# Performance work log

Measured on AMD Instinct MI355X. Metric: run time of the kernel, lower is better.

Reference implementation:

```python
import jax, jax.numpy as jnp
import numpy as np

B, S, D = 2, 2048, 1024
HEADS, HEAD_DIM = 16, 64

def setup_inputs() -> dict:
    key = jax.random.key(0)
    ks = jax.random.split(key, 5)
    sc = 0.02
    return {
        "hidden_states": jax.random.normal(ks[0], (B, S, D), jnp.float32),
        "Wq": jax.random.normal(ks[1], (D, HEADS * HEAD_DIM), jnp.float32) * sc,
        "Wk": jax.random.normal(ks[2], (D, HEADS * HEAD_DIM), jnp.float32) * sc,
        "Wv": jax.random.normal(ks[3], (D, HEADS * HEAD_DIM), jnp.float32) * sc,
        "Wo": jax.random.normal(ks[4], (HEADS * HEAD_DIM, D), jnp.float32) * sc,
        "bo": jnp.zeros((D,), jnp.float32),
    }

def reference(hidden_states, Wq, Wk, Wv, Wo, bo):
    b, s, _ = hidden_states.shape
    # QKV projections (no bias, as in diffusers Attention defaults)
    q = (hidden_states @ Wq).reshape(b, s, HEADS, HEAD_DIM).transpose(0, 2, 1, 3)
    k = (hidden_states @ Wk).reshape(b, s, HEADS, HEAD_DIM).transpose(0, 2, 1, 3)
    v = (hidden_states @ Wv).reshape(b, s, HEADS, HEAD_DIM).transpose(0, 2, 1, 3)
    scale = 1.0 / jnp.sqrt(jnp.asarray(HEAD_DIM, hidden_states.dtype))
    scores = jnp.einsum('bhqd,bhkd->bhqk', q, k) * scale  # full NxN scores
    attn = jax.nn.softmax(scores, axis=-1)
    out = jnp.einsum('bhqk,bhkd->bhqd', attn, v)
    out = out.transpose(0, 2, 1, 3).reshape(b, s, HEADS * HEAD_DIM)
    return out @ Wo + bo
```

## Files before the change

### kernel.cpp

```cpp
#include <hip/hip_runtime.h>

#define B_ 2
#define S_ 2048
#define D_ 1024
#define H_ 16
#define HD_ 64
#define M_ (B_ * S_)

typedef __attribute__((ext_vector_type(4))) float f32x4;
typedef __attribute__((ext_vector_type(16))) float f32x16;
typedef __attribute__((ext_vector_type(8))) short s16x8;
typedef unsigned short u16;
typedef unsigned int u32;

#define QSCALE 0.1803368801111204f

__device__ __forceinline__ u16 f2bf(float f) {
  unsigned u = __float_as_uint(f);
  u += 0x7fffu + ((u >> 16) & 1u);
  return (u16)(u >> 16);
}

__device__ __forceinline__ u32 cvtpk_bf16(float lo, float hi) {
  u32 r;
  asm("v_cvt_pk_bf16_f32 %0, %1, %2" : "=v"(r) : "v"(lo), "v"(hi));
  return r;
}

__device__ __forceinline__ void g2lds16(const u16* g, u16* l) {
  __builtin_amdgcn_global_load_lds((const __attribute__((address_space(1))) u32*)(g),
                                   (__attribute__((address_space(3))) u32*)(l), 16, 0, 0);
}

__global__ __launch_bounds__(256) void prep_kernel(
    const float* __restrict__ X, const float* __restrict__ Wq,
    const float* __restrict__ Wk, const float* __restrict__ Wv,
    const float* __restrict__ Wo, u16* __restrict__ Xb, u16* __restrict__ Wt0) {
  __shared__ float tile[32][33];
  const int id = blockIdx.x;
  if (id < 4096) {
    int i = (id * 256 + threadIdx.x) * 4;
    const float4 v = *(const float4*)(X + i);
    ushort4 o;
    o.x = f2bf(v.x); o.y = f2bf(v.y); o.z = f2bf(v.z); o.w = f2bf(v.w);
    *(ushort4*)(Xb + i) = o;
    return;
  }
  const int id2 = id - 4096;
  const int z = id2 >> 10;
  const float* W = (z == 0) ? Wq : (z == 1) ? Wk : (z == 2) ? Wv : Wo;
  u16* Wt = Wt0 + (size_t)z * (D_ * D_);
  const float sc = (z == 0) ? QSCALE : 1.0f;
  const int tx = threadIdx.x & 31, ty = threadIdx.x >> 5;
  const int c0 = (id2 & 31) * 32, r0 = ((id2 >> 5) & 31) * 32;
#pragma unroll
  for (int j = 0; j < 32; j += 8)
    tile[ty + j][tx] = W[(size_t)(r0 + ty + j) * D_ + c0 + tx];
  __syncthreads();
#pragma unroll
  for (int j = 0; j < 32; j += 8)
    Wt[(size_t)(c0 + ty + j) * D_ + r0 + tx] = f2bf(tile[tx][ty + j] * sc);
}

__global__ __launch_bounds__(256) void gemm_qkv_kernel(
    const u16* __restrict__ Xb, const u16* __restrict__ WqT,
    const u16* __restrict__ WkT, const u16* __restrict__ WvT,
    u16* __restrict__ Qb, u16* __restrict__ Kb, u16* __restrict__ Vt) {
  __shared__ u16 As[2][128 * 32];
  __shared__ u16 Bs[2][128 * 32];
  const int tid = threadIdx.x;
  const int lane = tid & 63, wid = tid >> 6;
  const int wr = wid >> 1, wc = wid & 1;
  const int l15 = lane & 15, l4 = lane >> 4;
  const int bm = blockIdx.x * 128;
  const int bn128 = blockIdx.y;
  const int sel = bn128 >> 3;
  const u16* Wt = (sel == 0) ? WqT : (sel == 1) ? WkT : WvT;
  const int bn = (bn128 & 7) * 128;
  const int r0 = lane >> 2;
  const int c0 = lane & 3;

#define GSTAGE(buf, kt)                                                          \
  do {                                                                           \
    _Pragma("unroll") for (int j = 0; j < 2; ++j) {                              \
      const int row = (wid * 2 + j) * 16 + r0;                                   \
      g2lds16(Xb + (size_t)(bm + row) * D_ + (kt) + c0 * 8,                      \
              &As[buf][(wid * 2 + j) * 512]);                                    \
      g2lds16(Wt + (size_t)(bn + row) * D_ + (kt) + c0 * 8,                      \
              &Bs[buf][(wid * 2 + j) * 512]);                                    \
    }                                                                            \
  } while (0)

  f32x4 acc[4][4] = {};
  GSTAGE(0, 0);
  __syncthreads();
  int cur = 0;
  for (int kt = 0; kt < D_; kt += 32) {
    GSTAGE(cur ^ 1, (kt + 32) & (D_ - 1));
    s16x8 af[4], bfr[4];
#pragma unroll
    for (int i = 0; i < 4; ++i) af[i] = *(const s16x8*)&As[cur][(wr * 64 + i * 16 + l15) * 32 + l4 * 8];
#pragma unroll
    for (int j = 0; j < 4; ++j) bfr[j] = *(const s16x8*)&Bs[cur][(wc * 64 + j * 16 + l15) * 32 + l4 * 8];
#pragma unroll
    for (int i = 0; i < 4; ++i)
#pragma unroll
      for (int j = 0; j < 4; ++j)
        acc[i][j] = __builtin_amdgcn_mfma_f32_16x16x32_bf16(af[i], bfr[j], acc[i][j], 0, 0, 0);
    __syncthreads();
    cur ^= 1;
  }
#undef GSTAGE
#pragma unroll
  for (int i = 0; i < 4; ++i)
#pragma unroll
    for (int j = 0; j < 4; ++j)
#pragma unroll
      for (int r = 0; r < 4; ++r) {
        int m = bm + wr * 64 + i * 16 + l4 * 4 + r;
        int n = bn + wc * 64 + j * 16 + l15;
        int bb = m >> 11, s = m & (S_ - 1);
        int h = n >> 6, d = n & 63;
        u16 v = f2bf(acc[i][j][r]);
        size_t bhsel = (size_t)bb * H_ + h;
        if (sel == 0)      Qb[(bhsel * S_ + s) * HD_ + d] = v;
        else if (sel == 1) Kb[(bhsel * S_ + s) * HD_ + d] = v;
        else               Vt[(bhsel * HD_ + d) * S_ + s] = v;
      }
}

__global__ __launch_bounds__(512, 2) void attn_kernel(
    const u16* __restrict__ Qb, const u16* __restrict__ Kb,
    const u16* __restrict__ Vt, u16* __restrict__ Ob) {
  __shared__ char smem_raw[65536];
  typedef u16 (*lds_t)[2][4096];
  lds_t Ks = (lds_t)smem_raw;
  lds_t Vs = (lds_t)(smem_raw + 32768);
  const int tid = threadIdx.x;
  const int lane = tid & 63, wid = tid >> 6;
  const int qg = wid & 3, half = wid >> 2;
  const int l31 = lane & 31, hi = lane >> 5;
  const int id = blockIdx.x;
  const int bh = (id & 7) * 4 + (id >> 6);
  const int qx = (id >> 3) & 7;
  const size_t kbase = (size_t)bh * S_ * HD_;
  const size_t vbase = (size_t)bh * HD_ * S_;
  const int q0 = qx * 256 + qg * 64;
  const int r0 = lane >> 3;
  const int cs = ((lane & 7) ^ r0) * 8;
  const int kv0 = half << 10;

#define STAGE(buf, kvv)                                                          \
  do {                                                                           \
    _Pragma("unroll") for (int j = 0; j < 2; ++j) {                              \
      const int row = (qg * 2 + j) * 8 + r0;                                     \
      g2lds16(Kb + kbase + (size_t)((kvv) + row) * HD_ + cs,                     \
              &Ks[half][buf][(qg * 2 + j) * 512]);                               \
      g2lds16(Vt + vbase + (size_t)row * S_ + (kvv) + cs,                        \
              &Vs[half][buf][(qg * 2 + j) * 512]);                               \
    }                                                                            \
  } while (0)

  STAGE(0, kv0);

  s16x8 aqA[4], aqB[4];
#pragma unroll
  for (int kc = 0; kc < 4; ++kc) {
    aqA[kc] = *(const s16x8*)(Qb + kbase + (size_t)(q0 + l31) * HD_ + kc * 16 + hi * 8);
    aqB[kc] = *(const s16x8*)(Qb + kbase + (size_t)(q0 + 32 + l31) * HD_ + kc * 16 + hi * 8);
  }

  f32x16 accA0 = {}, accA1 = {}, accB0 = {}, accB1 = {};
  float lsA = 0.f, lsB = 0.f;

  int choff[4];
#pragma unroll
  for (int c = 0; c < 4; ++c) choff[c] = ((c * 2 + hi) ^ (l31 & 7)) * 8;

  __syncthreads();

  for (int t = 0; t < 16; ++t) {
    const int buf = t & 1;
    STAGE(buf ^ 1, kv0 + (((t + 1) & 15) << 6));

    f32x16 sA0 = {}, sA1 = {}, sB0 = {}, sB1 = {};
    __builtin_amdgcn_s_setprio(1);
#pragma unroll
    for (int kc = 0; kc < 4; ++kc) {
      const s16x8 ka0 = *(const s16x8*)&Ks[half][buf][(l31) * 64 + choff[kc]];
      const s16x8 ka1 = *(const s16x8*)&Ks[half][buf][(32 + l31) * 64 + choff[kc]];
      sA0 = __builtin_amdgcn_mfma_f32_32x32x16_bf16(ka0, aqA[kc], sA0, 0, 0, 0);
      sB0 = __builtin_amdgcn_mfma_f32_32x32x16_bf16(ka0, aqB[kc], sB0, 0, 0, 0);
      sA1 = __builtin_amdgcn_mfma_f32_32x32x16_bf16(ka1, aqA[kc], sA1, 0, 0, 0);
      sB1 = __builtin_amdgcn_mfma_f32_32x32x16_bf16(ka1, aqB[kc], sB1, 0, 0, 0);
    }
    __builtin_amdgcn_s_setprio(0);

    float tA = 0.f, tB = 0.f;
#pragma unroll
    for (int r = 0; r < 16; ++r) {
      sA0[r] = __builtin_amdgcn_exp2f(sA0[r]);
      sA1[r] = __builtin_amdgcn_exp2f(sA1[r]);
      sB0[r] = __builtin_amdgcn_exp2f(sB0[r]);
      sB1[r] = __builtin_amdgcn_exp2f(sB1[r]);
      tA += sA0[r] + sA1[r];
      tB += sB0[r] + sB1[r];
    }
    lsA += tA;
    lsB += tB;

    s16x8 paA[4], paB[4];
#pragma unroll
    for (int c = 0; c < 4; ++c) {
      const int rr = (c & 1) * 8;
      u32 a0, a1, b0, b1;
      if (c < 2) {
        a0 = cvtpk_bf16(sA0[rr + 0], sA0[rr + 1]);
        a1 = cvtpk_bf16(sA0[rr + 2], sA0[rr + 3]);
        b0 = cvtpk_bf16(sA0[rr + 4], sA0[rr + 5]);
        b1 = cvtpk_bf16(sA0[rr + 6], sA0[rr + 7]);
      } else {
        a0 = cvtpk_bf16(sA1[rr + 0], sA1[rr + 1]);
        a1 = cvtpk_bf16(sA1[rr + 2], sA1[rr + 3]);
        b0 = cvtpk_bf16(sA1[rr + 4], sA1[rr + 5]);
        b1 = cvtpk_bf16(sA1[rr + 6], sA1[rr + 7]);
      }
      asm volatile("v_permlane32_swap_b32 %0, %1" : "+v"(a0), "+v"(b0));
      asm volatile("v_permlane32_swap_b32 %0, %1" : "+v"(a1), "+v"(b1));
      union { u32 u[4]; s16x8 v; } pk;
      pk.u[0] = a0; pk.u[1] = a1; pk.u[2] = b0; pk.u[3] = b1;
      paA[c] = pk.v;
    }
#pragma unroll
    for (int c = 0; c < 4; ++c) {
      const int rr = (c & 1) * 8;
      u32 a0, a1, b0, b1;
      if (c < 2) {
        a0 = cvtpk_bf16(sB0[rr + 0], sB0[rr + 1]);
        a1 = cvtpk_bf16(sB0[rr + 2], sB0[rr + 3]);
        b0 = cvtpk_bf16(sB0[rr + 4], sB0[rr + 5]);
        b1 = cvtpk_bf16(sB0[rr + 6], sB0[rr + 7]);
      } else {
        a0 = cvtpk_bf16(sB1[rr + 0], sB1[rr + 1]);
        a1 = cvtpk_bf16(sB1[rr + 2], sB1[rr + 3]);
        b0 = cvtpk_bf16(sB1[rr + 4], sB1[rr + 5]);
        b1 = cvtpk_bf16(sB1[rr + 6], sB1[rr + 7]);
      }
      asm volatile("v_permlane32_swap_b32 %0, %1" : "+v"(a0), "+v"(b0));
      asm volatile("v_permlane32_swap_b32 %0, %1" : "+v"(a1), "+v"(b1));
      union { u32 u[4]; s16x8 v; } pk;
      pk.u[0] = a0; pk.u[1] = a1; pk.u[2] = b0; pk.u[3] = b1;
      paB[c] = pk.v;
    }

    __builtin_amdgcn_s_setprio(1);
#pragma unroll
    for (int c = 0; c < 4; ++c) {
      const s16x8 vb0 = *(const s16x8*)&Vs[half][buf][(l31) * 64 + choff[c]];
      const s16x8 vb1 = *(const s16x8*)&Vs[half][buf][(32 + l31) * 64 + choff[c]];
      accA0 = __builtin_amdgcn_mfma_f32_32x32x16_bf16(paA[c], vb0, accA0, 0, 0, 0);
      accB0 = __builtin_amdgcn_mfma_f32_32x32x16_bf16(paB[c], vb0, accB0, 0, 0, 0);
      accA1 = __builtin_amdgcn_mfma_f32_32x32x16_bf16(paA[c], vb1, accA1, 0, 0, 0);
      accB1 = __builtin_amdgcn_mfma_f32_32x32x16_bf16(paB[c], vb1, accB1, 0, 0, 0);
    }
    __builtin_amdgcn_s_setprio(0);

    __syncthreads();
  }
#undef STAGE

  lsA += __shfl_xor(lsA, 32);
  lsB += __shfl_xor(lsB, 32);
  const int bb = bh >> 4, h = bh & 15;
  float (*MB)[64][33] = (float(*)[64][33])smem_raw;

  if (half) {
#pragma unroll
    for (int r = 0; r < 16; ++r) {
      MB[qg][lane][r] = accA0[r];
      MB[qg][lane][16 + r] = accA1[r];
    }
    MB[qg][lane][32] = lsA;
  }
  __syncthreads();
  if (!half) {
    lsA += MB[qg][lane][32];
#pragma unroll
    for (int r = 0; r < 16; ++r) {
      accA0[r] += MB[qg][lane][r];
      accA1[r] += MB[qg][lane][16 + r];
    }
#pragma unroll
    for (int r = 0; r < 16; ++r) {
      const int qrow = (r & 3) + 8 * (r >> 2) + 4 * hi;
      const float rinv = 1.0f / __shfl(lsA, qrow);
      const int q = q0 + qrow;
      Ob[(size_t)(bb * S_ + q) * (H_ * HD_) + h * HD_ + l31] = f2bf(accA0[r] * rinv);
      Ob[(size_t)(bb * S_ + q) * (H_ * HD_) + h * HD_ + 32 + l31] = f2bf(accA1[r] * rinv);
    }
  }
  __syncthreads();
  if (half) {
#pragma unroll
    for (int r = 0; r < 16; ++r) {
      MB[qg][lane][r] = accB0[r];
      MB[qg][lane][16 + r] = accB1[r];
    }
    MB[qg][lane][32] = lsB;
  }
  __syncthreads();
  if (!half) {
    lsB += MB[qg][lane][32];
#pragma unroll
    for (int r = 0; r < 16; ++r) {
      accB0[r] += MB[qg][lane][r];
      accB1[r] += MB[qg][lane][16 + r];
    }
#pragma unroll
    for (int r = 0; r < 16; ++r) {
      const int qrow = (r & 3) + 8 * (r >> 2) + 4 * hi;
      const float rinv = 1.0f / __shfl(lsB, qrow);
      const int q = q0 + 32 + qrow;
      Ob[(size_t)(bb * S_ + q) * (H_ * HD_) + h * HD_ + l31] = f2bf(accB0[r] * rinv);
      Ob[(size_t)(bb * S_ + q) * (H_ * HD_) + h * HD_ + 32 + l31] = f2bf(accB1[r] * rinv);
    }
  }
}

__global__ __launch_bounds__(256, 2) void gemm_o_kernel(
    const u16* __restrict__ A, const u16* __restrict__ Bt,
    const float* __restrict__ bias, float* __restrict__ C) {
  __shared__ u16 As[2][128 * 32];
  __shared__ u16 Bs[2][64 * 32];
  const int tid = threadIdx.x;
  const int lane = tid & 63, wid = tid >> 6;
  const int l15 = lane & 15, l4 = lane >> 4;
  const int bm = blockIdx.x * 128;
  const int bn = blockIdx.y * 64;
  const int r0 = lane >> 2;
  const int c0 = lane & 3;

#define GSTAGE(buf, kt)                                                          \
  do {                                                                           \
    _Pragma("unroll") for (int j = 0; j < 2; ++j) {                              \
      const int row = (wid * 2 + j) * 16 + r0;                                   \
      g2lds16(A + (size_t)(bm + row) * D_ + (kt) + c0 * 8,                       \
              &As[buf][(wid * 2 + j) * 512]);                                    \
    }                                                                            \
    g2lds16(Bt + (size_t)(bn + wid * 16 + r0) * D_ + (kt) + c0 * 8,              \
            &Bs[buf][wid * 512]);                                                \
  } while (0)

  f32x4 acc[2][4] = {};
  GSTAGE(0, 0);
  __syncthreads();
  int cur = 0;
  for (int kt = 0; kt < D_; kt += 32) {
    GSTAGE(cur ^ 1, (kt + 32) & (D_ - 1));
    s16x8 af[2], bfr[4];
#pragma unroll
    for (int i = 0; i < 2; ++i) af[i] = *(const s16x8*)&As[cur][(wid * 32 + i * 16 + l15) * 32 + l4 * 8];
#pragma unroll
    for (int j = 0; j < 4; ++j) bfr[j] = *(const s16x8*)&Bs[cur][(j * 16 + l15) * 32 + l4 * 8];
#pragma unroll
    for (int i = 0; i < 2; ++i)
#pragma unroll
      for (int j = 0; j < 4; ++j)
        acc[i][j] = __builtin_amdgcn_mfma_f32_16x16x32_bf16(af[i], bfr[j], acc[i][j], 0, 0, 0);
    __syncthreads();
    cur ^= 1;
  }
#undef GSTAGE
#pragma unroll
  for (int i = 0; i < 2; ++i)
#pragma unroll
    for (int j = 0; j < 4; ++j)
#pragma unroll
      for (int r = 0; r < 4; ++r) {
        int m = bm + wid * 32 + i * 16 + l4 * 4 + r;
        int n = bn + j * 16 + l15;
        C[(size_t)m * D_ + n] = acc[i][j][r] + bias[n];
      }
}

extern "C" void kernel_launch(void* const* d_in, const int* in_sizes, int n_in,
                              void* d_out, int out_size, void* d_ws, size_t ws_size,
                              hipStream_t stream) {
  const float* X  = (const float*)d_in[0];
  const float* Wq = (const float*)d_in[1];
  const float* Wk = (const float*)d_in[2];
  const float* Wv = (const float*)d_in[3];
  const float* Wo = (const float*)d_in[4];
  const float* bo = (const float*)d_in[5];
  float* out = (float*)d_out;

  char* w = (char*)d_ws;
  u16* Xb  = (u16*)(w);
  u16* WT  = (u16*)(w + (8u << 20));
  u16* WqT = WT;
  u16* WkT = WT + (1u << 20);
  u16* WvT = WT + (2u << 20);
  u16* WoT = WT + (3u << 20);
  u16* Qb  = (u16*)(w + (16u << 20));
  u16* Kb  = (u16*)(w + (24u << 20));
  u16* Vt  = (u16*)(w + (32u << 20));
  u16* Ob  = (u16*)(w + (40u << 20));

  prep_kernel<<<8192, 256, 0, stream>>>(X, Wq, Wk, Wv, Wo, Xb, WT);
  gemm_qkv_kernel<<<dim3(32, 24), 256, 0, stream>>>(Xb, WqT, WkT, WvT, Qb, Kb, Vt);
  attn_kernel<<<256, 512, 0, stream>>>(Qb, Kb, Vt, Ob);
  gemm_o_kernel<<<dim3(32, 16), 256, 0, stream>>>(Ob, WoT, bo, out);
}
```

Measured before the change: 113.8 us.

## Split attention KV range four ways across 1024-thread blocks

The attention kernel doubles its block size to 16 waves. Each group of four waves now handles a quarter of the KV sequence (8 tiles) instead of half (16 tiles), using 128KB of LDS for the K/V double buffers. Partial accumulators and row sums from the three extra quarters are merged through LDS at the end. This adds per-CU parallelism and shortens the serial KV loop, at the cost of a larger final reduction. The launch bound of (1024, 4) may also force a tighter register budget and cause spills.

```diff
diff --git a/kernel.cpp b/kernel.cpp
--- a/kernel.cpp
+++ b/kernel.cpp
@@ -129,16 +129,16 @@
       }
 }
 
-__global__ __launch_bounds__(512, 2) void attn_kernel(
+__global__ __launch_bounds__(1024, 4) void attn_kernel(
     const u16* __restrict__ Qb, const u16* __restrict__ Kb,
     const u16* __restrict__ Vt, u16* __restrict__ Ob) {
-  __shared__ char smem_raw[65536];
+  __shared__ char smem_raw[131072];
   typedef u16 (*lds_t)[2][4096];
   lds_t Ks = (lds_t)smem_raw;
-  lds_t Vs = (lds_t)(smem_raw + 32768);
+  lds_t Vs = (lds_t)(smem_raw + 65536);
   const int tid = threadIdx.x;
   const int lane = tid & 63, wid = tid >> 6;
-  const int qg = wid & 3, half = wid >> 2;
+  const int qg = wid & 3, quarter = wid >> 2;
   const int l31 = lane & 31, hi = lane >> 5;
   const int id = blockIdx.x;
   const int bh = (id & 7) * 4 + (id >> 6);
@@ -148,16 +148,16 @@
   const int q0 = qx * 256 + qg * 64;
   const int r0 = lane >> 3;
   const int cs = ((lane & 7) ^ r0) * 8;
-  const int kv0 = half << 10;
+  const int kv0 = quarter << 9;
 
 #define STAGE(buf, kvv)                                                          \
   do {                                                                           \
     _Pragma("unroll") for (int j = 0; j < 2; ++j) {                              \
       const int row = (qg * 2 + j) * 8 + r0;                                     \
       g2lds16(Kb + kbase + (size_t)((kvv) + row) * HD_ + cs,                     \
-              &Ks[half][buf][(qg * 2 + j) * 512]);                               \
+              &Ks[quarter][buf][(qg * 2 + j) * 512]);                            \
       g2lds16(Vt + vbase + (size_t)row * S_ + (kvv) + cs,                        \
-              &Vs[half][buf][(qg * 2 + j) * 512]);                               \
+              &Vs[quarter][buf][(qg * 2 + j) * 512]);                            \
     }                                                                            \
   } while (0)
 
@@ -179,16 +179,16 @@
 
   __syncthreads();
 
-  for (int t = 0; t < 16; ++t) {
+  for (int t = 0; t < 8; ++t) {
     const int buf = t & 1;
-    STAGE(buf ^ 1, kv0 + (((t + 1) & 15) << 6));
+    STAGE(buf ^ 1, kv0 + (((t + 1) & 7) << 6));
 
     f32x16 sA0 = {}, sA1 = {}, sB0 = {}, sB1 = {};
     __builtin_amdgcn_s_setprio(1);
 #pragma unroll
     for (int kc = 0; kc < 4; ++kc) {
-      const s16x8 ka0 = *(const s16x8*)&Ks[half][buf][(l31) * 64 + choff[kc]];
-      const s16x8 ka1 = *(const s16x8*)&Ks[half][buf][(32 + l31) * 64 + choff[kc]];
+      const s16x8 ka0 = *(const s16x8*)&Ks[quarter][buf][(l31) * 64 + choff[kc]];
+      const s16x8 ka1 = *(const s16x8*)&Ks[quarter][buf][(32 + l31) * 64 + choff[kc]];
       sA0 = __builtin_amdgcn_mfma_f32_32x32x16_bf16(ka0, aqA[kc], sA0, 0, 0, 0);
       sB0 = __builtin_amdgcn_mfma_f32_32x32x16_bf16(ka0, aqB[kc], sB0, 0, 0, 0);
       sA1 = __builtin_amdgcn_mfma_f32_32x32x16_bf16(ka1, aqA[kc], sA1, 0, 0, 0);
@@ -256,8 +256,8 @@
     __builtin_amdgcn_s_setprio(1);
 #pragma unroll
     for (int c = 0; c < 4; ++c) {
-      const s16x8 vb0 = *(const s16x8*)&Vs[half][buf][(l31) * 64 + choff[c]];
-      const s16x8 vb1 = *(const s16x8*)&Vs[half][buf][(32 + l31) * 64 + choff[c]];
+      const s16x8 vb0 = *(const s16x8*)&Vs[quarter][buf][(l31) * 64 + choff[c]];
+      const s16x8 vb1 = *(const s16x8*)&Vs[quarter][buf][(32 + l31) * 64 + choff[c]];
       accA0 = __builtin_amdgcn_mfma_f32_32x32x16_bf16(paA[c], vb0, accA0, 0, 0, 0);
       accB0 = __builtin_amdgcn_mfma_f32_32x32x16_bf16(paB[c], vb0, accB0, 0, 0, 0);
       accA1 = __builtin_amdgcn_mfma_f32_32x32x16_bf16(paA[c], vb1, accA1, 0, 0, 0);
@@ -272,54 +272,54 @@
   lsA += __shfl_xor(lsA, 32);
   lsB += __shfl_xor(lsB, 32);
   const int bb = bh >> 4, h = bh & 15;
-  float (*MB)[64][33] = (float(*)[64][33])smem_raw;
-
-  if (half) {
-#pragma unroll
-    for (int r = 0; r < 16; ++r) {
-      MB[qg][lane][r] = accA0[r];
-      MB[qg][lane][16 + r] = accA1[r];
-    }
-    MB[qg][lane][32] = lsA;
-  }
-  __syncthreads();
-  if (!half) {
-    lsA += MB[qg][lane][32];
-#pragma unroll
-    for (int r = 0; r < 16; ++r) {
-      accA0[r] += MB[qg][lane][r];
-      accA1[r] += MB[qg][lane][16 + r];
+  float (*MB)[4][64][33] = (float(*)[4][64][33])smem_raw;
+
+  if (quarter) {
+#pragma unroll
+    for (int r = 0; r < 16; ++r) {
+      MB[quarter - 1][qg][lane][r] = accA0[r];
+      MB[quarter - 1][qg][lane][16 + r] = accA1[r];
+    }
+    MB[quarter - 1][qg][lane][32] = lsA;
+  }
+  __syncthreads();
+  if (!quarter) {
+    float ls = lsA + MB[0][qg][lane][32] + MB[1][qg][lane][32] + MB[2][qg][lane][32];
+#pragma unroll
+    for (int r = 0; r < 16; ++r) {
+      accA0[r] += MB[0][qg][lane][r] + MB[1][qg][lane][r] + MB[2][qg][lane][r];
+      accA1[r] += MB[0][qg][lane][16 + r] + MB[1][qg][lane][16 + r] + MB[2][qg][lane][16 + r];
     }
 #pragma unroll
     for (int r = 0; r < 16; ++r) {
       const int qrow = (r & 3) + 8 * (r >> 2) + 4 * hi;
-      const float rinv = 1.0f / __shfl(lsA, qrow);
+      const float rinv = 1.0f / __shfl(ls, qrow);
       const int q = q0 + qrow;
       Ob[(size_t)(bb * S_ + q) * (H_ * HD_) + h * HD_ + l31] = f2bf(accA0[r] * rinv);
       Ob[(size_t)(bb * S_ + q) * (H_ * HD_) + h * HD_ + 32 + l31] = f2bf(accA1[r] * rinv);
     }
   }
   __syncthreads();
-  if (half) {
-#pragma unroll
-    for (int r = 0; r < 16; ++r) {
-      MB[qg][lane][r] = accB0[r];
-      MB[qg][lane][16 + r] = accB1[r];
-    }
-    MB[qg][lane][32] = lsB;
-  }
-  __syncthreads();
-  if (!half) {
-    lsB += MB[qg][lane][32];
-#pragma unroll
-    for (int r = 0; r < 16; ++r) {
-      accB0[r] += MB[qg][lane][r];
-      accB1[r] += MB[qg][lane][16 + r];
+  if (quarter) {
+#pragma unroll
+    for (int r = 0; r < 16; ++r) {
+      MB[quarter - 1][qg][lane][r] = accB0[r];
+      MB[quarter - 1][qg][lane][16 + r] = accB1[r];
+    }
+    MB[quarter - 1][qg][lane][32] = lsB;
+  }
+  __syncthreads();
+  if (!quarter) {
+    float ls = lsB + MB[0][qg][lane][32] + MB[1][qg][lane][32] + MB[2][qg][lane][32];
+#pragma unroll
+    for (int r = 0; r < 16; ++r) {
+      accB0[r] += MB[0][qg][lane][r] + MB[1][qg][lane][r] + MB[2][qg][lane][r];
+      accB1[r] += MB[0][qg][lane][16 + r] + MB[1][qg][lane][16 + r] + MB[2][qg][lane][16 + r];
     }
 #pragma unroll
     for (int r = 0; r < 16; ++r) {
       const int qrow = (r & 3) + 8 * (r >> 2) + 4 * hi;
-      const float rinv = 1.0f / __shfl(lsB, qrow);
+      const float rinv = 1.0f / __shfl(ls, qrow);
       const int q = q0 + 32 + qrow;
       Ob[(size_t)(bb * S_ + q) * (H_ * HD_) + h * HD_ + l31] = f2bf(accB0[r] * rinv);
       Ob[(size_t)(bb * S_ + q) * (H_ * HD_) + h * HD_ + 32 + l31] = f2bf(accB1[r] * rinv);
@@ -408,6 +408,6 @@
 
   prep_kernel<<<8192, 256, 0, stream>>>(X, Wq, Wk, Wv, Wo, Xb, WT);
   gemm_qkv_kernel<<<dim3(32, 24), 256, 0, stream>>>(Xb, WqT, WkT, WvT, Qb, Kb, Vt);
-  attn_kernel<<<256, 512, 0, stream>>>(Qb, Kb, Vt, Ob);
+  attn_kernel<<<256, 1024, 0, stream>>>(Qb, Kb, Vt, Ob);
   gemm_o_kernel<<<dim3(32, 16), 256, 0, stream>>>(Ob, WoT, bo, out);
 }
```

Result: slower. 284.8 us (+150.4%).
